# Performance work log

Measured on AMD Instinct MI355X. Metric: run time of the kernel, lower is better.

Reference implementation:

```python
import jax, jax.numpy as jnp
import numpy as np

BN_EPS = 1e-5
ALPHA = 0.3
NEG = -9e9
BN_SCALE = 1.0 / np.sqrt(1.0 + BN_EPS)  # eval BatchNorm with running_mean=0, running_var=1


def gat_layer(x, mask, W, a, bn_g, bn_b, concat):
    # x: [B,N,Fin], mask: [B,N,N] bool, W: [Fin,Fo], a: [2*Fo]
    h = jnp.einsum('bnf,fo->bno', x, W)               # [B,N,Fo]
    Fo = W.shape[1]
    s1 = h @ a[:Fo]                                    # [B,N]
    s2 = h @ a[Fo:]                                    # [B,N]
    # additive decomposition of concat([h_i, h_j]) @ a (identical math)
    e = jax.nn.leaky_relu(s1[:, :, None] + s2[:, None, :], ALPHA)  # [B,N,N]
    att = jax.nn.softmax(jnp.where(mask, e, NEG), axis=-1)
    hp = jnp.einsum('bnm,bmo->bno', att, h)            # [B,N,Fo]
    # BatchNorm1d(nodes_num) in eval mode, per-node-channel affine
    hp = hp * BN_SCALE * bn_g[None, :, None] + bn_b[None, :, None]
    return jax.nn.elu(hp) if concat else hp


def setup_inputs() -> dict:
    key = jax.random.key(0)
    ks = jax.random.split(key, 10)
    B, N, F, Fo, H, C = 128, 200, 768, 32, 8, 2
    Fh = Fo * H
    return {
        'feat_matrix': jax.random.normal(ks[0], (B, N, F), jnp.float32),
        'adj': jax.random.randint(ks[1], (B, N, N), 0, 2, jnp.int32),
        'W_heads': jax.random.normal(ks[2], (H, F, Fo), jnp.float32) * 0.05,
        'a_heads': jax.random.normal(ks[3], (H, 2 * Fo), jnp.float32) * 0.1,
        'bnh_g': jnp.ones((H, N), jnp.float32),
        'bnh_b': jnp.zeros((H, N), jnp.float32),
        'bnt_g': jnp.ones((N,), jnp.float32),
        'bnt_b': jnp.zeros((N,), jnp.float32),
        'W_sent': jax.random.normal(ks[4], (Fh, C), jnp.float32) * 0.1,
        'a_sent': jax.random.normal(ks[5], (2 * C,), jnp.float32) * 0.1,
        'bns_g': jnp.ones((N,), jnp.float32),
        'bns_b': jnp.zeros((N,), jnp.float32),
        'W_para': jax.random.normal(ks[6], (Fh, C), jnp.float32) * 0.1,
        'a_para': jax.random.normal(ks[7], (2 * C,), jnp.float32) * 0.1,
        'bnp_g': jnp.ones((N,), jnp.float32),
        'bnp_b': jnp.zeros((N,), jnp.float32),
        'W_q': jax.random.normal(ks[8], (Fh, Fo), jnp.float32) * 0.1,
        'a_q': jax.random.normal(ks[9], (2 * Fo,), jnp.float32) * 0.1,
        'bnq_g': jnp.ones((N,), jnp.float32),
        'bnq_b': jnp.zeros((N,), jnp.float32),
        'W2': jax.random.normal(jax.random.fold_in(key, 99), (Fo, 2), jnp.float32) * 0.1,
    }


def reference(feat_matrix, adj, W_heads, a_heads, bnh_g, bnh_b, bnt_g, bnt_b,
              W_sent, a_sent, bns_g, bns_b, W_para, a_para, bnp_g, bnp_b,
              W_q, a_q, bnq_g, bnq_b, W2):
    mask = adj > 0
    # 8 attention heads (concat=True), vmapped over head dim
    heads = jax.vmap(lambda W, a, g, b: gat_layer(feat_matrix, mask, W, a, g, b, True))(
        W_heads, a_heads, bnh_g, bnh_b)              # [H,B,N,Fo]
    H, B, N, Fo = heads.shape
    x = jnp.moveaxis(heads, 0, 2).reshape(B, N, H * Fo)  # head-major concat, matches torch.cat
    # top-level BatchNorm1d (eval) + dropout(no-op)
    x = x * BN_SCALE * bnt_g[None, :, None] + bnt_b[None, :, None]
    logits_sent = jax.nn.sigmoid(gat_layer(x, mask, W_sent, a_sent, bns_g, bns_b, False))
    logits_para = jax.nn.elu(gat_layer(x, mask, W_para, a_para, bnp_g, bnp_b, False))
    q = gat_layer(x, mask, W_q, a_q, bnq_g, bnq_b, False)[:, 0, :]   # [B,Fo]
    logits_Qtype = jax.nn.elu(q @ W2).reshape(-1, 2)
    return (logits_sent, logits_para, logits_Qtype)
```

## Files before the change

kernel.cpp:

```cpp
#include <hip/hip_runtime.h>
#include <hip/hip_bf16.h>
#include <cstdint>

#define BN_SCALEF 0.99999500003749975f
#define EXP_SHIFT 4.0f


typedef _Float16 half8 __attribute__((ext_vector_type(8)));
typedef _Float16 half4 __attribute__((ext_vector_type(4)));
typedef float floatx4 __attribute__((ext_vector_type(4)));


__global__ __launch_bounds__(256) void prep(const int* __restrict__ adj,
                                            const float* __restrict__ W_heads,
                                            const float* __restrict__ Ws_in,
                                            const float* __restrict__ Wp_in,
                                            const float* __restrict__ Wq_in,
                                            const float* __restrict__ a_sent,
                                            const float* __restrict__ a_para,
                                            const float* __restrict__ a_q,
                                            unsigned int* __restrict__ maskw,
                                            _Float16* __restrict__ Bt,
                                            _Float16* __restrict__ W2t48) {
    int blk = blockIdx.x;
    int t = threadIdx.x;
    if (blk < 1600) {
        int w = t >> 6, lane = t & 63;
        for (int task = w; task < 64; task += 4) {
            int r = blk * 16 + (task >> 2);
            int c0 = (task & 3) * 64;
            int j = c0 + lane;
            bool v = (j < 200) && (adj[(size_t)r * 200 + j] > 0);
            unsigned long long m = __ballot(v ? 1 : 0);
            if (lane == 0) {
                maskw[r * 8 + (c0 >> 5)]     = (unsigned int)(m & 0xffffffffULL);
                maskw[r * 8 + (c0 >> 5) + 1] = (unsigned int)(m >> 32);
            }
        }
    } else if (blk < 1792) {
        __shared__ float ld[32][36];
        int blk2 = blk - 1600;
        int h = blk2 / 24, f0 = (blk2 % 24) * 32;
        int idx = t * 4;
        int fr = idx >> 5, o0 = idx & 31;
        float4 v = *(const float4*)&W_heads[(size_t)h * 24576 + (size_t)(f0 + fr) * 32 + o0];
        ld[fr][o0] = v.x; ld[fr][o0 + 1] = v.y; ld[fr][o0 + 2] = v.z; ld[fr][o0 + 3] = v.w;
        __syncthreads();
        int o = idx >> 5, fr0 = idx & 31;
        half4 hv;
#pragma unroll
        for (int u = 0; u < 4; ++u) hv[u] = (_Float16)ld[fr0 + u][o];
        *(half4*)&Bt[(size_t)(h * 32 + o) * 768 + f0 + fr0] = hv;
    } else {
        int k = t;
        for (int c = 0; c < 36; ++c) {
            float v;
            if (c < 2)      v = Ws_in[k * 2 + c];
            else if (c < 4) v = Wp_in[k * 2 + (c - 2)];
            else            v = Wq_in[k * 32 + (c - 4)];
            W2t48[c * 256 + k] = (_Float16)v;
        }
        W2t48[36 * 256 + k] = (_Float16)(Ws_in[k * 2] * a_sent[0] + Ws_in[k * 2 + 1] * a_sent[1]);
        W2t48[37 * 256 + k] = (_Float16)(Ws_in[k * 2] * a_sent[2] + Ws_in[k * 2 + 1] * a_sent[3]);
        W2t48[38 * 256 + k] = (_Float16)(Wp_in[k * 2] * a_para[0] + Wp_in[k * 2 + 1] * a_para[1]);
        W2t48[39 * 256 + k] = (_Float16)(Wp_in[k * 2] * a_para[2] + Wp_in[k * 2 + 1] * a_para[3]);
        float q1 = 0.f, q2 = 0.f;
#pragma unroll
        for (int o = 0; o < 32; ++o) {
            q1 += Wq_in[k * 32 + o] * a_q[o];
            q2 += Wq_in[k * 32 + o] * a_q[32 + o];
        }
        W2t48[40 * 256 + k] = (_Float16)q1;
        W2t48[41 * 256 + k] = (_Float16)q2;
        for (int c = 42; c < 48; ++c) W2t48[c * 256 + k] = (_Float16)0.f;
    }
}


__global__ __launch_bounds__(512) void gemm1_mfma(const float* __restrict__ A,
                                                  const _Float16* __restrict__ Bt,
                                                  _Float16* __restrict__ h16) {
    __shared__ __align__(16) _Float16 As[64 * 40];
    __shared__ __align__(16) _Float16 Bs[256 * 40];
    int t = threadIdx.x;
    int m0 = blockIdx.x * 64;
    int w = t >> 6, lane = t & 63;
    int wr = w >> 2, wc = w & 3;
    int quad = lane >> 4, l16 = lane & 15;

    floatx4 acc[2][4];
#pragma unroll
    for (int i = 0; i < 2; ++i)
#pragma unroll
        for (int j = 0; j < 4; ++j) acc[i][j] = (floatx4){0.f, 0.f, 0.f, 0.f};

    int arow = t >> 3, ako = (t & 7) * 4;
    int bcol = t >> 1, bko = (t & 1) * 16;
    const float*    Aptr = &A[(size_t)(m0 + arow) * 768 + ako];
    const _Float16* Bptr = &Bt[(size_t)bcol * 768 + bko];

    float4 pa  = *(const float4*)(Aptr);
    uint4  pb0 = *(const uint4*)(Bptr);
    uint4  pb1 = *(const uint4*)(Bptr + 8);

    for (int k0 = 0; k0 < 768; k0 += 32) {
        half4 ah;
        ah[0] = (_Float16)pa.x; ah[1] = (_Float16)pa.y;
        ah[2] = (_Float16)pa.z; ah[3] = (_Float16)pa.w;
        *(half4*)&As[arow * 40 + ako] = ah;
        *(uint4*)&Bs[bcol * 40 + bko]     = pb0;
        *(uint4*)&Bs[bcol * 40 + bko + 8] = pb1;
        __syncthreads();
        if (k0 + 32 < 768) {
            pa  = *(const float4*)(Aptr + k0 + 32);
            pb0 = *(const uint4*)(Bptr + k0 + 32);
            pb1 = *(const uint4*)(Bptr + k0 + 40);
        }
        half8 af[2], bf[4];
#pragma unroll
        for (int rt = 0; rt < 2; ++rt)
            af[rt] = *(half8*)&As[(wr * 32 + rt * 16 + l16) * 40 + quad * 8];
#pragma unroll
        for (int ct = 0; ct < 4; ++ct)
            bf[ct] = *(half8*)&Bs[(wc * 64 + ct * 16 + l16) * 40 + quad * 8];
#pragma unroll
        for (int rt = 0; rt < 2; ++rt)
#pragma unroll
            for (int ct = 0; ct < 4; ++ct)
                acc[rt][ct] = __builtin_amdgcn_mfma_f32_16x16x32_f16(af[rt], bf[ct], acc[rt][ct], 0, 0, 0);
        __syncthreads();
    }

    int rbase = m0 + wr * 32;
    int cbase = wc * 64;
#pragma unroll
    for (int rt = 0; rt < 2; ++rt)
#pragma unroll
        for (int ct = 0; ct < 4; ++ct) {
            int gc = cbase + ct * 16 + l16;
#pragma unroll
            for (int r = 0; r < 4; ++r) {
                int gr = rbase + rt * 16 + quad * 4 + r;
                h16[(size_t)gr * 256 + gc] = (_Float16)acc[rt][ct][r];
            }
        }
}


__global__ __launch_bounds__(256) void attn_heads_mfma(
    const _Float16* __restrict__ h16,
    const float* __restrict__ a_h,
    const unsigned int* __restrict__ maskw,
    const float* __restrict__ bnh_g, const float* __restrict__ bnh_b,
    const float* __restrict__ bnt_g, const float* __restrict__ bnt_b,
    _Float16* __restrict__ x16h) {
    __shared__ __align__(16) _Float16 Bs[32 * 228];
    __shared__ __align__(16) _Float16 Bs2[16 * 228];
    __shared__ __align__(16) _Float16 Ps[64 * 228];
    __shared__ float s1s[256], s2s[256];
    unsigned int* Ms = (unsigned int*)((char*)Bs2 + 512);
    int hb = blockIdx.x;
    int h = hb >> 7, b = hb & 127;
    int t = threadIdx.x;

    unsigned long long* bz = (unsigned long long*)Bs;
    for (int idx = t; idx < (32 * 228) / 4; idx += 256) bz[idx] = 0ULL;
    unsigned long long* bz2 = (unsigned long long*)Bs2;
    for (int idx = t; idx < (16 * 228) / 4; idx += 256) bz2[idx] = 0ULL;
    __syncthreads();
    for (int idx = t; idx < 800; idx += 256) {
        int j = idx >> 2, w8 = (idx & 3) * 8;
        half8 v = *(const half8*)&h16[(size_t)(b * 200 + j) * 256 + h * 32 + w8];
#pragma unroll
        for (int u = 0; u < 8; ++u) Bs[(w8 + u) * 228 + j] = v[u];
    }
    if (t < 200) Bs2[t] = (_Float16)1.0f;
    for (int idx = t; idx < 400; idx += 256)
        *(uint4*)&Ms[idx * 4] = *(const uint4*)&maskw[(size_t)b * 1600 + idx * 4];
    __syncthreads();

    if (t < 200) {
        float acc1 = 0.f, acc2 = 0.f;
        const float* ab = &a_h[h * 64];
#pragma unroll
        for (int o = 0; o < 32; ++o) {
            float hv = (float)Bs[o * 228 + t];
            acc1 += hv * ab[o];
            acc2 += hv * ab[32 + o];
        }
        s1s[t] = acc1; s2s[t] = acc2;
    } else {
        s1s[t] = 0.f; s2s[t] = 0.f;
    }
    __syncthreads();

    int w = t >> 6, lane = t & 63;
    int l16 = lane & 15, quad = lane >> 4;
    _Float16* Pw = &Ps[w * 16 * 228];

    int j0 = lane * 4;
    float4 s2r = *(const float4*)&s2s[j0];
    int mword = lane >> 3;

    for (int tile = w; tile < 13; tile += 4) {
        int i_base = tile * 16;
        for (int r16 = 0; r16 < 16; ++r16) {
            int i = i_base + r16;
            int ic = i < 200 ? i : 199;
            unsigned int mw = Ms[ic * 8 + mword];
            float s1v = s1s[i];
            half4 pv;
#pragma unroll
            for (int q = 0; q < 4; ++q) {
                float e = s1v + ((const float*)&s2r)[q];
                e = fmaxf(e, 0.3f * e);
                float p = ((mw >> ((j0 + q) & 31)) & 1u) ? __expf(e - EXP_SHIFT) : 0.f;
                pv[q] = (_Float16)p;
            }
            if (j0 < 228) *(half4*)&Pw[r16 * 228 + j0] = pv;
        }
        floatx4 acc0 = {0.f, 0.f, 0.f, 0.f};
        floatx4 acc1 = {0.f, 0.f, 0.f, 0.f};
        floatx4 acc2 = {0.f, 0.f, 0.f, 0.f};
#pragma unroll
        for (int kt = 0; kt < 7; ++kt) {
            half8 af = *(half8*)&Pw[l16 * 228 + kt * 32 + quad * 8];
            half8 b0 = *(half8*)&Bs[(l16) * 228 + kt * 32 + quad * 8];
            half8 b1 = *(half8*)&Bs[(16 + l16) * 228 + kt * 32 + quad * 8];
            half8 b2 = *(half8*)&Bs2[(l16) * 228 + kt * 32 + quad * 8];
            acc0 = __builtin_amdgcn_mfma_f32_16x16x32_f16(af, b0, acc0, 0, 0, 0);
            acc1 = __builtin_amdgcn_mfma_f32_16x16x32_f16(af, b1, acc1, 0, 0, 0);
            acc2 = __builtin_amdgcn_mfma_f32_16x16x32_f16(af, b2, acc2, 0, 0, 0);
        }
#pragma unroll
        for (int r = 0; r < 4; ++r) {
            int i = i_base + quad * 4 + r;
            float rsum = __shfl(acc2[r], (lane & 48), 64);
            if (i < 200) {
                float inv = 1.f / rsum;
                float g1 = BN_SCALEF * bnh_g[h * 200 + i], c1 = bnh_b[h * 200 + i];
                float g2 = BN_SCALEF * bnt_g[i], c2 = bnt_b[i];
                float v0 = acc0[r] * inv * g1 + c1;
                v0 = v0 > 0.f ? v0 : __expf(v0) - 1.f;
                v0 = v0 * g2 + c2;
                float v1 = acc1[r] * inv * g1 + c1;
                v1 = v1 > 0.f ? v1 : __expf(v1) - 1.f;
                v1 = v1 * g2 + c2;
                size_t base = (size_t)h * 819200 + (size_t)(b * 200 + i) * 32;
                x16h[base + l16]      = (_Float16)v0;
                x16h[base + 16 + l16] = (_Float16)v1;
            }
        }
    }
}


__global__ __launch_bounds__(256) void gemm2m(const _Float16* __restrict__ Xh,
                                              const _Float16* __restrict__ Wt,
                                              float* __restrict__ H2p) {
    __shared__ __align__(16) _Float16 Xs[64 * 264];
    __shared__ __align__(16) _Float16 Ws[48 * 264];
    int t = threadIdx.x;
    int m0 = blockIdx.x * 64;
    int srow = t >> 2, schunk = (t & 3) * 8;
#pragma unroll
    for (int h = 0; h < 8; ++h) {
        half8 v = *(const half8*)&Xh[(size_t)h * 819200 + (size_t)(m0 + srow) * 32 + schunk];
        *(half8*)&Xs[srow * 264 + h * 32 + schunk] = v;
    }
#pragma unroll
    for (int p = 0; p < 6; ++p) {
        int g = t + 256 * p;
        int n = g >> 5, ko = (g & 31) * 8;
        *(half8*)&Ws[n * 264 + ko] = *(const half8*)&Wt[(size_t)n * 256 + ko];
    }
    __syncthreads();

    int w = t >> 6, lane = t & 63;
    int l16 = lane & 15, quad = lane >> 4;
    int rbase = w * 16;
    floatx4 acc[3];
#pragma unroll
    for (int c = 0; c < 3; ++c) acc[c] = (floatx4){0.f, 0.f, 0.f, 0.f};
#pragma unroll
    for (int kt = 0; kt < 8; ++kt) {
        half8 af = *(half8*)&Xs[(rbase + l16) * 264 + kt * 32 + quad * 8];
#pragma unroll
        for (int ct = 0; ct < 3; ++ct) {
            half8 bf = *(half8*)&Ws[(ct * 16 + l16) * 264 + kt * 32 + quad * 8];
            acc[ct] = __builtin_amdgcn_mfma_f32_16x16x32_f16(af, bf, acc[ct], 0, 0, 0);
        }
    }
#pragma unroll
    for (int ct = 0; ct < 3; ++ct) {
        int col = ct * 16 + l16;
#pragma unroll
        for (int r = 0; r < 4; ++r) {
            int row = m0 + rbase + quad * 4 + r;
            H2p[(size_t)row * 48 + col] = acc[ct][r];
        }
    }
}


__global__ __launch_bounds__(256) void attn_spq(const float* __restrict__ H2p,
                                                const unsigned int* __restrict__ maskw,
                                                const float* __restrict__ bns_g, const float* __restrict__ bns_b,
                                                const float* __restrict__ bnp_g, const float* __restrict__ bnp_b,
                                                const float* __restrict__ bnq_g, const float* __restrict__ bnq_b,
                                                const float* __restrict__ W2, float* __restrict__ out) {
    int b = blockIdx.x;
    int t = threadIdx.x;
    if (blockIdx.y == 2) {
        __shared__ float p_lds[200];
        __shared__ float redd[4];
        __shared__ float red2[256];
        float s1v = H2p[(size_t)(b * 200) * 48 + 40];
        float p = 0.f;
        if (t < 200) {
            unsigned int mw = maskw[(size_t)(b * 200) * 8 + (t >> 5)];
            if ((mw >> (t & 31)) & 1u) {
                float x = s1v + H2p[(size_t)(b * 200 + t) * 48 + 41];
                x = fmaxf(x, 0.3f * x);
                p = __expf(x - EXP_SHIFT);
            }
            p_lds[t] = p;
        }
        float ds = p;
        for (int off = 32; off; off >>= 1) ds += __shfl_xor(ds, off, 64);
        if ((t & 63) == 0) redd[t >> 6] = ds;
        __syncthreads();
        ds = redd[0] + redd[1] + redd[2] + redd[3];
        int o = t & 31, g = t >> 5;
        float acc = 0.f;
        for (int j = g; j < 200; j += 8)
            acc += p_lds[j] * H2p[(size_t)(b * 200 + j) * 48 + 4 + o];
        red2[t] = acc;
        __syncthreads();
        if (t < 32) {
            float s = 0.f;
#pragma unroll
            for (int gg = 0; gg < 8; ++gg) s += red2[gg * 32 + t];
            float qv = (s / ds) * (BN_SCALEF * bnq_g[0]) + bnq_b[0];
            float c0 = qv * W2[t * 2], c1 = qv * W2[t * 2 + 1];
#pragma unroll
            for (int off = 16; off; off >>= 1) {
                c0 += __shfl_xor(c0, off, 64);
                c1 += __shfl_xor(c1, off, 64);
            }
            if (t == 0) {
                out[102400 + b * 2 + 0] = c0 > 0.f ? c0 : __expf(c0) - 1.f;
                out[102400 + b * 2 + 1] = c1 > 0.f ? c1 : __expf(c1) - 1.f;
            }
        }
        return;
    }
    __shared__ float s2s[200], s2p[200];
    __shared__ float s1sA[200], s1pA[200];
    __shared__ __align__(16) float hsp[200 * 4];
    __shared__ __align__(16) unsigned int Msq[800];
    int chunk = blockIdx.y;
    if (t < 200) {
        const float* hr = &H2p[(size_t)(b * 200 + t) * 48];
        float4 hv = *(const float4*)hr;
        *(float4*)&hsp[t * 4] = hv;
        s1sA[t] = hr[36]; s2s[t] = hr[37];
        s1pA[t] = hr[38]; s2p[t] = hr[39];
    }
    for (int idx = t; idx < 200; idx += 256)
        *(uint4*)&Msq[idx * 4] = *(const uint4*)&maskw[((size_t)(b * 200) + chunk * 100) * 8 + idx * 4];
    __syncthreads();
    int w = t >> 6, lane = t & 63;
    for (int it = 0; it < 25; ++it) {
        int i = chunk * 100 + it * 4 + w;
        float s1sv = s1sA[i];
        float s1pv = s1pA[i];
        float ds = 0.f, dp = 0.f, pa0 = 0.f, pa1 = 0.f, pb0 = 0.f, pb1 = 0.f;
#pragma unroll
        for (int q = 0; q < 4; ++q) {
            int j = lane + 64 * q;
            if (j < 200) {
                unsigned int mw = Msq[(it * 4 + w) * 8 + (j >> 5)];
                if ((mw >> (j & 31)) & 1u) {
                    float x1 = s1sv + s2s[j]; x1 = fmaxf(x1, 0.3f * x1);
                    float x2 = s1pv + s2p[j]; x2 = fmaxf(x2, 0.3f * x2);
                    float p1 = __expf(x1 - EXP_SHIFT), p2 = __expf(x2 - EXP_SHIFT);
                    ds += p1; dp += p2;
                    float4 hv = *(float4*)&hsp[j * 4];
                    pa0 += p1 * hv.x; pa1 += p1 * hv.y;
                    pb0 += p2 * hv.z; pb1 += p2 * hv.w;
                }
            }
        }
        for (int off = 32; off; off >>= 1) {
            ds  += __shfl_xor(ds, off, 64);  dp  += __shfl_xor(dp, off, 64);
            pa0 += __shfl_xor(pa0, off, 64); pa1 += __shfl_xor(pa1, off, 64);
            pb0 += __shfl_xor(pb0, off, 64); pb1 += __shfl_xor(pb1, off, 64);
        }
        if (lane == 0) {
            float gs = BN_SCALEF * bns_g[i], bs = bns_b[i];
            float v0 = (pa0 / ds) * gs + bs, v1 = (pa1 / ds) * gs + bs;
            out[(size_t)(b * 200 + i) * 2 + 0] = 1.f / (1.f + __expf(-v0));
            out[(size_t)(b * 200 + i) * 2 + 1] = 1.f / (1.f + __expf(-v1));
            float gp = BN_SCALEF * bnp_g[i], bp = bnp_b[i];
            float u0 = (pb0 / dp) * gp + bp, u1 = (pb1 / dp) * gp + bp;
            out[51200 + (size_t)(b * 200 + i) * 2 + 0] = u0 > 0.f ? u0 : __expf(u0) - 1.f;
            out[51200 + (size_t)(b * 200 + i) * 2 + 1] = u1 > 0.f ? u1 : __expf(u1) - 1.f;
        }
    }
}


extern "C" void kernel_launch(void* const* d_in, const int* in_sizes, int n_in,
                              void* d_out, int out_size, void* d_ws, size_t ws_size,
                              hipStream_t stream) {
    (void)in_sizes; (void)n_in; (void)out_size; (void)ws_size;
    const float* feat    = (const float*)d_in[0];
    const int*   adj     = (const int*)d_in[1];
    const float* W_heads = (const float*)d_in[2];
    const float* a_heads = (const float*)d_in[3];
    const float* bnh_g   = (const float*)d_in[4];
    const float* bnh_b   = (const float*)d_in[5];
    const float* bnt_g   = (const float*)d_in[6];
    const float* bnt_b   = (const float*)d_in[7];
    const float* W_sent  = (const float*)d_in[8];
    const float* a_sent  = (const float*)d_in[9];
    const float* bns_g   = (const float*)d_in[10];
    const float* bns_b   = (const float*)d_in[11];
    const float* W_para  = (const float*)d_in[12];
    const float* a_para  = (const float*)d_in[13];
    const float* bnp_g   = (const float*)d_in[14];
    const float* bnp_b   = (const float*)d_in[15];
    const float* W_q     = (const float*)d_in[16];
    const float* a_q     = (const float*)d_in[17];
    const float* bnq_g   = (const float*)d_in[18];
    const float* bnq_b   = (const float*)d_in[19];
    const float* W2      = (const float*)d_in[20];
    float* out = (float*)d_out;
    float* ws  = (float*)d_ws;

    _Float16* h16   = (_Float16*)ws;
    _Float16* x16h  = (_Float16*)(ws + 3276800);
    _Float16* W2t48 = (_Float16*)(ws + 6553600);
    _Float16* Bt    = (_Float16*)(ws + 6559744);
    unsigned int* maskw = (unsigned int*)(ws + 6658048);
    float* H2p   = ws + 6862848;

    prep<<<dim3(1793), dim3(256), 0, stream>>>(adj, W_heads, W_sent, W_para, W_q,
                                               a_sent, a_para, a_q, maskw, Bt, W2t48);
    gemm1_mfma<<<dim3(400), dim3(512), 0, stream>>>(feat, Bt, h16);
    attn_heads_mfma<<<dim3(1024), dim3(256), 0, stream>>>(h16, a_heads, maskw,
                                                          bnh_g, bnh_b, bnt_g, bnt_b, x16h);
    gemm2m<<<dim3(400), dim3(256), 0, stream>>>(x16h, W2t48, H2p);
    attn_spq<<<dim3(128, 3), dim3(256), 0, stream>>>(H2p, maskw, bns_g, bns_b,
                                                     bnp_g, bnp_b, bnq_g, bnq_b, W2, out);
}
```

Measured before the change: 275.2 us.

## Spread mask packing over one block per row and stage W_q via LDS

The mask-packing part of the prep kernel now launches one block per adjacency row, 25600 blocks in total, with each of the four waves handling one 64-column chunk. Before, 1600 blocks each looped over 16 rows. The change is meant to expose more memory-level parallelism when reading the 13 MB int adjacency. The single weight-packing block now loads W_q into padded shared memory so column reads are coalesced instead of strided. The cost is many more tiny blocks, which adds launch and scheduling overhead.

```diff
diff --git a/kernel.cpp b/kernel.cpp
--- a/kernel.cpp
+++ b/kernel.cpp
@@ -24,22 +24,20 @@
                                             _Float16* __restrict__ W2t48) {
     int blk = blockIdx.x;
     int t = threadIdx.x;
-    if (blk < 1600) {
+    if (blk < 25600) {
         int w = t >> 6, lane = t & 63;
-        for (int task = w; task < 64; task += 4) {
-            int r = blk * 16 + (task >> 2);
-            int c0 = (task & 3) * 64;
-            int j = c0 + lane;
-            bool v = (j < 200) && (adj[(size_t)r * 200 + j] > 0);
-            unsigned long long m = __ballot(v ? 1 : 0);
-            if (lane == 0) {
-                maskw[r * 8 + (c0 >> 5)]     = (unsigned int)(m & 0xffffffffULL);
-                maskw[r * 8 + (c0 >> 5) + 1] = (unsigned int)(m >> 32);
-            }
-        }
-    } else if (blk < 1792) {
+        int r = blk;
+        int c0 = w * 64;
+        int j = c0 + lane;
+        bool v = (j < 200) && (adj[(size_t)r * 200 + j] > 0);
+        unsigned long long m = __ballot(v ? 1 : 0);
+        if (lane == 0) {
+            maskw[r * 8 + (c0 >> 5)]     = (unsigned int)(m & 0xffffffffULL);
+            maskw[r * 8 + (c0 >> 5) + 1] = (unsigned int)(m >> 32);
+        }
+    } else if (blk < 25792) {
         __shared__ float ld[32][36];
-        int blk2 = blk - 1600;
+        int blk2 = blk - 25600;
         int h = blk2 / 24, f0 = (blk2 % 24) * 32;
         int idx = t * 4;
         int fr = idx >> 5, o0 = idx & 31;
@@ -52,23 +50,32 @@
         for (int u = 0; u < 4; ++u) hv[u] = (_Float16)ld[fr0 + u][o];
         *(half4*)&Bt[(size_t)(h * 32 + o) * 768 + f0 + fr0] = hv;
     } else {
+        __shared__ float WqL[32 * 257];
+        for (int i = t; i < 8192; i += 256) {
+            int kk = i >> 5, oo = i & 31;
+            WqL[oo * 257 + kk] = Wq_in[i];
+        }
+        __syncthreads();
         int k = t;
-        for (int c = 0; c < 36; ++c) {
-            float v;
-            if (c < 2)      v = Ws_in[k * 2 + c];
-            else if (c < 4) v = Wp_in[k * 2 + (c - 2)];
-            else            v = Wq_in[k * 32 + (c - 4)];
-            W2t48[c * 256 + k] = (_Float16)v;
-        }
-        W2t48[36 * 256 + k] = (_Float16)(Ws_in[k * 2] * a_sent[0] + Ws_in[k * 2 + 1] * a_sent[1]);
-        W2t48[37 * 256 + k] = (_Float16)(Ws_in[k * 2] * a_sent[2] + Ws_in[k * 2 + 1] * a_sent[3]);
-        W2t48[38 * 256 + k] = (_Float16)(Wp_in[k * 2] * a_para[0] + Wp_in[k * 2 + 1] * a_para[1]);
-        W2t48[39 * 256 + k] = (_Float16)(Wp_in[k * 2] * a_para[2] + Wp_in[k * 2 + 1] * a_para[3]);
+        float w0 = Ws_in[k * 2], w1 = Ws_in[k * 2 + 1];
+        float p0 = Wp_in[k * 2], p1 = Wp_in[k * 2 + 1];
+        W2t48[0 * 256 + k] = (_Float16)w0;
+        W2t48[1 * 256 + k] = (_Float16)w1;
+        W2t48[2 * 256 + k] = (_Float16)p0;
+        W2t48[3 * 256 + k] = (_Float16)p1;
+#pragma unroll
+        for (int c = 4; c < 36; ++c)
+            W2t48[c * 256 + k] = (_Float16)WqL[(c - 4) * 257 + k];
+        W2t48[36 * 256 + k] = (_Float16)(w0 * a_sent[0] + w1 * a_sent[1]);
+        W2t48[37 * 256 + k] = (_Float16)(w0 * a_sent[2] + w1 * a_sent[3]);
+        W2t48[38 * 256 + k] = (_Float16)(p0 * a_para[0] + p1 * a_para[1]);
+        W2t48[39 * 256 + k] = (_Float16)(p0 * a_para[2] + p1 * a_para[3]);
         float q1 = 0.f, q2 = 0.f;
 #pragma unroll
         for (int o = 0; o < 32; ++o) {
-            q1 += Wq_in[k * 32 + o] * a_q[o];
-            q2 += Wq_in[k * 32 + o] * a_q[32 + o];
+            float wv = WqL[o * 257 + k];
+            q1 += wv * a_q[o];
+            q2 += wv * a_q[32 + o];
         }
         W2t48[40 * 256 + k] = (_Float16)q1;
         W2t48[41 * 256 + k] = (_Float16)q2;
@@ -446,8 +453,8 @@
     unsigned int* maskw = (unsigned int*)(ws + 6658048);
     float* H2p   = ws + 6862848;
 
-    prep<<<dim3(1793), dim3(256), 0, stream>>>(adj, W_heads, W_sent, W_para, W_q,
-                                               a_sent, a_para, a_q, maskw, Bt, W2t48);
+    prep<<<dim3(25793), dim3(256), 0, stream>>>(adj, W_heads, W_sent, W_para, W_q,
+                                                a_sent, a_para, a_q, maskw, Bt, W2t48);
     gemm1_mfma<<<dim3(400), dim3(512), 0, stream>>>(feat, Bt, h16);
     attn_heads_mfma<<<dim3(1024), dim3(256), 0, stream>>>(h16, a_heads, maskw,
                                                           bnh_g, bnh_b, bnt_g, bnt_b, x16h);
```

After: 283.8 us. 3.1% more time.
